# Performance work log

Hardware: AMD Instinct MI355X
Metric: run time of the kernel (lower is better)

Reference implementation:

```python
import jax, jax.numpy as jnp
import numpy as np

N_CLASSES = 91  # classes 0..90; class 0 (background) is excluded from the mean


def setup_inputs() -> dict:
    key = jax.random.key(0)
    k1, k2 = jax.random.split(key)
    B, H, W = 64, 512, 512
    # label maps with integer class ids in [0, 91); `inputs` stored as float32
    # to mirror the original (compared elementwise against integer i)
    inputs = jax.random.randint(k1, (B, H, W), 0, N_CLASSES).astype(jnp.float32)
    targets = jax.random.randint(k2, (B, H, W), 0, N_CLASSES).astype(jnp.int32)
    return {"inputs": inputs, "targets": targets, "smooth": 1}


def reference(inputs, targets, smooth):
    # Single-pass histogram formulation of the original per-class loop:
    #   intersection_i = #{p : inputs[p]==i and targets[p]==i}
    #   total_i        = #{inputs==i} + #{targets==i}
    #   union_i        = total_i - intersection_i
    n = N_CLASSES
    inp = inputs.reshape(-1).astype(jnp.int32)
    tgt = targets.reshape(-1).astype(jnp.int32)
    cnt_in = jnp.bincount(inp, length=n).astype(jnp.float32)
    cnt_tg = jnp.bincount(tgt, length=n).astype(jnp.float32)
    # positions where prediction == target contribute to that class's intersection;
    # mismatches are routed to a dummy bin n and dropped
    inter = jnp.bincount(jnp.where(inp == tgt, inp, n), length=n + 1)[:n].astype(jnp.float32)
    union = cnt_in + cnt_tg - inter
    smooth_f = jnp.float32(smooth)
    iou = (inter[1:] + smooth_f) / (union[1:] + smooth_f)  # classes 1..n-1
    return jnp.sum(iou) / (n - 1)
```

## Files before the change

### kernel.cpp

```cpp
#include <hip/hip_runtime.h>

#define NCLS 91
#define NHIST (3 * NCLS)
#define NBLK 2048
#define BS 256
#define NWAVE (BS / 64)

__device__ __forceinline__ void process4(unsigned int* hw, float4 fv, int4 tv) {
    int a0 = (int)fv.x, a1 = (int)fv.y, a2 = (int)fv.z, a3 = (int)fv.w;
    atomicAdd(&hw[a0], 1u);
    atomicAdd(&hw[a1], 1u);
    atomicAdd(&hw[a2], 1u);
    atomicAdd(&hw[a3], 1u);
    atomicAdd(&hw[NCLS + tv.x], 1u);
    atomicAdd(&hw[NCLS + tv.y], 1u);
    atomicAdd(&hw[NCLS + tv.z], 1u);
    atomicAdd(&hw[NCLS + tv.w], 1u);
    if (a0 == tv.x) atomicAdd(&hw[2 * NCLS + a0], 1u);
    if (a1 == tv.y) atomicAdd(&hw[2 * NCLS + a1], 1u);
    if (a2 == tv.z) atomicAdd(&hw[2 * NCLS + a2], 1u);
    if (a3 == tv.w) atomicAdd(&hw[2 * NCLS + a3], 1u);
}

__global__ __launch_bounds__(BS) void miou_hist(const float* __restrict__ inp,
                                                const int* __restrict__ tgt,
                                                unsigned int* __restrict__ ws,
                                                int n4) {
    __shared__ unsigned int h[NWAVE][NHIST];
    for (int i = threadIdx.x; i < NWAVE * NHIST; i += BS)
        ((unsigned int*)h)[i] = 0u;
    __syncthreads();

    unsigned int* hw = h[threadIdx.x >> 6];

    int tid = blockIdx.x * BS + threadIdx.x;
    int stride = gridDim.x * BS;
    const float4* in4 = (const float4*)inp;
    const int4* tg4 = (const int4*)tgt;

    int i = tid;
    for (; i + 3 * stride < n4; i += 4 * stride) {
        float4 f0 = in4[i];
        float4 f1 = in4[i + stride];
        float4 f2 = in4[i + 2 * stride];
        float4 f3 = in4[i + 3 * stride];
        int4 t0 = tg4[i];
        int4 t1 = tg4[i + stride];
        int4 t2 = tg4[i + 2 * stride];
        int4 t3 = tg4[i + 3 * stride];
        process4(hw, f0, t0);
        process4(hw, f1, t1);
        process4(hw, f2, t2);
        process4(hw, f3, t3);
    }
    for (; i < n4; i += stride) process4(hw, in4[i], tg4[i]);
    __syncthreads();

    for (int i2 = threadIdx.x; i2 < NHIST; i2 += BS) {
        unsigned int v = 0u;
        #pragma unroll
        for (int w = 0; w < NWAVE; ++w) v += h[w][i2];
        if (v) atomicAdd(&ws[i2], v);
    }
}

__global__ void miou_finalize(const unsigned int* __restrict__ ws,
                              const int* __restrict__ smooth_p,
                              float* __restrict__ out) {
    int lane = threadIdx.x;
    float s = (float)(*smooth_p);
    float acc = 0.f;
    for (int c = 1 + lane; c < NCLS; c += 64) {
        float ci = (float)ws[c];
        float ct = (float)ws[NCLS + c];
        float it = (float)ws[2 * NCLS + c];
        float un = ci + ct - it;
        acc += (it + s) / (un + s);
    }
    #pragma unroll
    for (int off = 32; off; off >>= 1) acc += __shfl_down(acc, off);
    if (lane == 0) out[0] = acc / (float)(NCLS - 1);
}

extern "C" void kernel_launch(void* const* d_in, const int* in_sizes, int n_in,
                              void* d_out, int out_size, void* d_ws, size_t ws_size,
                              hipStream_t stream) {
    const float* inp = (const float*)d_in[0];
    const int* tgt = (const int*)d_in[1];
    const int* smooth_p = (const int*)d_in[2];
    float* out = (float*)d_out;
    unsigned int* ws = (unsigned int*)d_ws;

    int n = in_sizes[0];
    int n4 = n >> 2;

    hipMemsetAsync(ws, 0, NHIST * sizeof(unsigned int), stream);
    miou_hist<<<NBLK, BS, 0, stream>>>(inp, tgt, ws, n4);
    miou_finalize<<<1, 64, 0, stream>>>(ws, smooth_p, out);
}
```

Baseline: 162.5 us.

## Replace three per-wave histograms with a joint pair histogram in LDS

Instead of three separate atomic histograms per element, each (pred, target) pair is counted once in a 91x91 joint histogram in shared memory, and the row sums, column sums and diagonal are derived at block end. This cuts LDS atomics from up to three per element to one and spreads them over 8281 bins, which lowers contention. The grid and block sizes also change to 1024 blocks of 512 threads, and the loop unroll drops from 4 to 2. In exchange the per-wave privatization is gone, the end-of-block reduction is a longer serial loop, and the larger LDS footprint (about 33 KB) may limit how many blocks fit per CU.

New measurement: 167.3 us. +3.0%, slower.

```diff
diff --git a/kernel.cpp b/kernel.cpp
--- a/kernel.cpp
+++ b/kernel.cpp
@@ -1,37 +1,26 @@
 #include <hip/hip_runtime.h>
 
 #define NCLS 91
+#define NP (NCLS * NCLS)
 #define NHIST (3 * NCLS)
-#define NBLK 2048
-#define BS 256
-#define NWAVE (BS / 64)
+#define NBLK 1024
+#define BS 512
 
-__device__ __forceinline__ void process4(unsigned int* hw, float4 fv, int4 tv) {
-    int a0 = (int)fv.x, a1 = (int)fv.y, a2 = (int)fv.z, a3 = (int)fv.w;
-    atomicAdd(&hw[a0], 1u);
-    atomicAdd(&hw[a1], 1u);
-    atomicAdd(&hw[a2], 1u);
-    atomicAdd(&hw[a3], 1u);
-    atomicAdd(&hw[NCLS + tv.x], 1u);
-    atomicAdd(&hw[NCLS + tv.y], 1u);
-    atomicAdd(&hw[NCLS + tv.z], 1u);
-    atomicAdd(&hw[NCLS + tv.w], 1u);
-    if (a0 == tv.x) atomicAdd(&hw[2 * NCLS + a0], 1u);
-    if (a1 == tv.y) atomicAdd(&hw[2 * NCLS + a1], 1u);
-    if (a2 == tv.z) atomicAdd(&hw[2 * NCLS + a2], 1u);
-    if (a3 == tv.w) atomicAdd(&hw[2 * NCLS + a3], 1u);
+__device__ __forceinline__ void proc4(unsigned int* __restrict__ ph, float4 f, int4 t) {
+    int a0 = (int)f.x, a1 = (int)f.y, a2 = (int)f.z, a3 = (int)f.w;
+    atomicAdd(&ph[a0 * NCLS + t.x], 1u);
+    atomicAdd(&ph[a1 * NCLS + t.y], 1u);
+    atomicAdd(&ph[a2 * NCLS + t.z], 1u);
+    atomicAdd(&ph[a3 * NCLS + t.w], 1u);
 }
 
-__global__ __launch_bounds__(BS) void miou_hist(const float* __restrict__ inp,
-                                                const int* __restrict__ tgt,
-                                                unsigned int* __restrict__ ws,
-                                                int n4) {
-    __shared__ unsigned int h[NWAVE][NHIST];
-    for (int i = threadIdx.x; i < NWAVE * NHIST; i += BS)
-        ((unsigned int*)h)[i] = 0u;
+__global__ __launch_bounds__(BS, 8) void miou_hist(const float* __restrict__ inp,
+                                                   const int* __restrict__ tgt,
+                                                   unsigned int* __restrict__ ws,
+                                                   int n4) {
+    __shared__ unsigned int ph[NP];
+    for (int i = threadIdx.x; i < NP; i += BS) ph[i] = 0u;
     __syncthreads();
-
-    unsigned int* hw = h[threadIdx.x >> 6];
 
     int tid = blockIdx.x * BS + threadIdx.x;
     int stride = gridDim.x * BS;
@@ -39,28 +28,32 @@
     const int4* tg4 = (const int4*)tgt;
 
     int i = tid;
-    for (; i + 3 * stride < n4; i += 4 * stride) {
+    for (; i + stride < n4; i += 2 * stride) {
         float4 f0 = in4[i];
+        int4 t0 = tg4[i];
         float4 f1 = in4[i + stride];
-        float4 f2 = in4[i + 2 * stride];
-        float4 f3 = in4[i + 3 * stride];
-        int4 t0 = tg4[i];
         int4 t1 = tg4[i + stride];
-        int4 t2 = tg4[i + 2 * stride];
-        int4 t3 = tg4[i + 3 * stride];
-        process4(hw, f0, t0);
-        process4(hw, f1, t1);
-        process4(hw, f2, t2);
-        process4(hw, f3, t3);
+        proc4(ph, f0, t0);
+        proc4(ph, f1, t1);
     }
-    for (; i < n4; i += stride) process4(hw, in4[i], tg4[i]);
+    if (i < n4) proc4(ph, in4[i], tg4[i]);
     __syncthreads();
 
-    for (int i2 = threadIdx.x; i2 < NHIST; i2 += BS) {
-        unsigned int v = 0u;
-        #pragma unroll
-        for (int w = 0; w < NWAVE; ++w) v += h[w][i2];
-        if (v) atomicAdd(&ws[i2], v);
+    int t = threadIdx.x;
+    if (t < NCLS) {
+        unsigned int s = 0;
+        const unsigned int* p = ph + t * NCLS;
+        for (int k = 0; k < NCLS; ++k) s += p[k];
+        if (s) atomicAdd(&ws[t], s);
+    } else if (t >= 128 && t < 128 + NCLS) {
+        int c = t - 128;
+        unsigned int s = 0;
+        for (int a = 0; a < NCLS; ++a) s += ph[a * NCLS + c];
+        if (s) atomicAdd(&ws[NCLS + c], s);
+    } else if (t >= 256 && t < 256 + NCLS) {
+        int d = t - 256;
+        unsigned int v = ph[d * (NCLS + 1)];
+        if (v) atomicAdd(&ws[2 * NCLS + d], v);
     }
 }
 
```
